# Kernel optimization log

Hardware: AMD Instinct MI355X
Metric: run time of the kernel (lower is better)

Reference implementation:

```python
import jax, jax.numpy as jnp
import numpy as np

NUM_HEADS = 16

def setup_inputs() -> dict:
    key = jax.random.key(0)
    k1, k2, k3, k4 = jax.random.split(key, 4)
    B, N, C = 4, 2048, 1024
    x = jax.random.normal(k1, (B, N, C), dtype=jnp.float32)
    xpos = jax.random.randint(k2, (B, N), 0, 2048, dtype=jnp.int64)
    Wqkv = jax.random.normal(k3, (C, 3 * C), dtype=jnp.float32) * (C ** -0.5)
    Wproj = jax.random.normal(k4, (C, C), dtype=jnp.float32) * (C ** -0.5)
    bproj = jnp.zeros((C,), dtype=jnp.float32)
    return {"x": x, "xpos": xpos, "Wqkv": Wqkv, "Wproj": Wproj, "bproj": bproj}

def reference(x, xpos, Wqkv, Wproj, bproj):
    # rope is None in this configuration, so xpos is unused (matches torch default path).
    B, N, C = x.shape
    H = NUM_HEADS
    Dh = C // H
    scale = Dh ** -0.5
    qkv = jnp.einsum('bnc,cd->bnd', x, Wqkv)              # [B, N, 3C]
    qkv = qkv.reshape(B, N, 3, H, Dh)
    q, k, v = qkv[:, :, 0], qkv[:, :, 1], qkv[:, :, 2]    # [B, N, H, Dh]
    scores = jnp.einsum('bnhd,bmhd->bhnm', q, k) * scale  # [B, H, N, N]
    attn = jax.nn.softmax(scores, axis=-1)
    out = jnp.einsum('bhnm,bmhd->bnhd', attn, v)          # [B, N, H, Dh]
    out = out.reshape(B, N, C)
    return jnp.einsum('bnc,cd->bnd', out, Wproj) + bproj
```

## Files before the change

kernel.cpp:

```cpp
#include <hip/hip_runtime.h>
#include <stdint.h>

#define DEVINL __device__ __forceinline__

typedef __bf16 bf16x8 __attribute__((ext_vector_type(8)));
typedef float f32x4 __attribute__((ext_vector_type(4)));
typedef float f32x16 __attribute__((ext_vector_type(16)));
typedef uint32_t u32x4 __attribute__((ext_vector_type(4)));

DEVINL uint16_t f2bf(float f) {
    uint32_t u = __builtin_bit_cast(uint32_t, f);
    uint32_t r = (u + 0x7FFFu + ((u >> 16) & 1u)) >> 16;
    return (uint16_t)r;
}

DEVINL bf16x8 ld8(const uint16_t* p) {
    u32x4 v = *(const u32x4*)p;
    return __builtin_bit_cast(bf16x8, v);
}

DEVINL void gload16(const void* g, void* l) {
    __builtin_amdgcn_global_load_lds(
        (const __attribute__((address_space(1))) uint32_t*)g,
        (__attribute__((address_space(3))) uint32_t*)l, 16, 0, 0);
}

DEVINL uint32_t cvtpk(float lo, float hi) {
    uint32_t r;
    asm("v_cvt_pk_bf16_f32 %0, %1, %2" : "=v"(r) : "v"(lo), "v"(hi));
    return r;
}

DEVINL float exp2_fast(float x) {
    float r;
    asm("v_exp_f32 %0, %1" : "=v"(r) : "v"(x));
    return r;
}

__global__ void k_cvt_x(const float* __restrict__ x, uint16_t* __restrict__ xb, int n8) {
    int i = blockIdx.x * blockDim.x + threadIdx.x;
    if (i >= n8) return;
    const float4* src = (const float4*)x + (size_t)i * 2;
    float4 a = src[0], b = src[1];
    union { uint16_t u[8]; u32x4 v; } o;
    o.u[0] = f2bf(a.x); o.u[1] = f2bf(a.y); o.u[2] = f2bf(a.z); o.u[3] = f2bf(a.w);
    o.u[4] = f2bf(b.x); o.u[5] = f2bf(b.y); o.u[6] = f2bf(b.z); o.u[7] = f2bf(b.w);
    ((u32x4*)xb)[i] = o.v;
}

__global__ void k_transW(const float* __restrict__ W, uint16_t* __restrict__ WT, int Nn) {
    __shared__ uint16_t t[64 * 65];
    int k0 = blockIdx.y * 64, n0 = blockIdx.x * 64;
    int tid = threadIdx.x;
#pragma unroll
    for (int i = 0; i < 4; ++i) {
        int c = tid + i * 256;
        int kr = c >> 4, nc = c & 15;
        float4 v = *(const float4*)(W + (size_t)(k0 + kr) * Nn + n0 + nc * 4);
        t[(nc * 4 + 0) * 65 + kr] = f2bf(v.x);
        t[(nc * 4 + 1) * 65 + kr] = f2bf(v.y);
        t[(nc * 4 + 2) * 65 + kr] = f2bf(v.z);
        t[(nc * 4 + 3) * 65 + kr] = f2bf(v.w);
    }
    __syncthreads();
#pragma unroll
    for (int i = 0; i < 2; ++i) {
        int c = tid + i * 256;
        int nr = c >> 3, kc = c & 7;
        union { uint16_t u[8]; u32x4 v; } o;
#pragma unroll
        for (int j = 0; j < 8; ++j) o.u[j] = t[nr * 65 + kc * 8 + j];
        *(u32x4*)(WT + (size_t)(n0 + nr) * 1024 + k0 + kc * 8) = o.v;
    }
}

__global__ void k_transV(const uint16_t* __restrict__ vn, uint16_t* __restrict__ vt) {
    __shared__ uint16_t t[64 * 65];
    int bh = blockIdx.y;
    int n0 = blockIdx.x * 64;
    int tid = threadIdx.x;
#pragma unroll
    for (int i = 0; i < 2; ++i) {
        int c = tid + i * 256;
        int n = c >> 3, dc = c & 7;
        u32x4 vv = *(const u32x4*)(vn + ((size_t)bh * 2048 + n0 + n) * 64 + dc * 8);
        union { u32x4 v4; uint16_t u[8]; } in; in.v4 = vv;
#pragma unroll
        for (int j = 0; j < 8; ++j) t[(dc * 8 + j) * 65 + n] = in.u[j];
    }
    __syncthreads();
#pragma unroll
    for (int i = 0; i < 2; ++i) {
        int c = tid + i * 256;
        int dh = c >> 3, nc = c & 7;
        union { uint16_t u[8]; u32x4 v4; } o;
#pragma unroll
        for (int j = 0; j < 8; ++j) o.u[j] = t[dh * 65 + nc * 8 + j];
        *(u32x4*)(vt + ((size_t)bh * 64 + dh) * 2048 + n0 + nc * 8) = o.v4;
    }
}

template <int MODE>
__global__ __launch_bounds__(256) void k_gemm(
    const uint16_t* __restrict__ A, const uint16_t* __restrict__ BT,
    const float* __restrict__ bias,
    uint16_t* __restrict__ qo, uint16_t* __restrict__ ko, uint16_t* __restrict__ vo,
    float* __restrict__ out) {
    __shared__ uint16_t a_lds[128 * 64];
    __shared__ uint16_t b_lds[128 * 64];
    int tid = threadIdx.x;
    int w = tid >> 6, l = tid & 63;
    int l15 = l & 15, l4 = l >> 4;
    int m0 = blockIdx.y * 128, n0 = blockIdx.x * 128;
    int wr = w >> 1, wc = w & 1;
    f32x4 acc[4][4] = {};

    for (int kt = 0; kt < 16; ++kt) {
#pragma unroll
        for (int i = 0; i < 4; ++i) {
            int c = i * 256 + w * 64 + l;
            int row = c >> 3, slot = c & 7;
            int kc = slot ^ (row & 7);
            gload16(A + (size_t)(m0 + row) * 1024 + kt * 64 + kc * 8,
                    a_lds + (size_t)(i * 256 + w * 64) * 8);
            gload16(BT + (size_t)(n0 + row) * 1024 + kt * 64 + kc * 8,
                    b_lds + (size_t)(i * 256 + w * 64) * 8);
        }
        __syncthreads();
#pragma unroll
        for (int kkk = 0; kkk < 2; ++kkk) {
            bf16x8 af[4], bfr[4];
#pragma unroll
            for (int i = 0; i < 4; ++i) {
                int row = wr * 64 + i * 16 + l15;
                af[i] = ld8(a_lds + row * 64 + ((kkk * 4 + l4) ^ (row & 7)) * 8);
                int rowb = wc * 64 + i * 16 + l15;
                bfr[i] = ld8(b_lds + rowb * 64 + ((kkk * 4 + l4) ^ (rowb & 7)) * 8);
            }
#pragma unroll
            for (int i = 0; i < 4; ++i)
#pragma unroll
                for (int j = 0; j < 4; ++j)
                    acc[i][j] = __builtin_amdgcn_mfma_f32_16x16x32_bf16(
                        af[i], bfr[j], acc[i][j], 0, 0, 0);
        }
        __syncthreads();
    }

    if constexpr (MODE == 0) {
#pragma unroll
        for (int i = 0; i < 4; ++i)
#pragma unroll
            for (int j = 0; j < 4; ++j) {
                int d = n0 + wc * 64 + j * 16 + l15;
                int s = d >> 10, h = (d >> 6) & 15, dh = d & 63;
                uint16_t* dst0 = (s == 0) ? qo : (s == 1) ? ko : vo;
                float sc = (s == 0) ? 0.18033688011112042f : 1.0f;
#pragma unroll
                for (int r = 0; r < 4; ++r) {
                    int m = m0 + wr * 64 + i * 16 + l4 * 4 + r;
                    int b = m >> 11, n = m & 2047;
                    dst0[((size_t)(b * 16 + h) * 2048 + n) * 64 + dh] = f2bf(acc[i][j][r] * sc);
                }
            }
    } else {
#pragma unroll
        for (int j = 0; j < 4; ++j) {
            int d = n0 + wc * 64 + j * 16 + l15;
            float bv = bias[d];
#pragma unroll
            for (int i = 0; i < 4; ++i)
#pragma unroll
                for (int r = 0; r < 4; ++r) {
                    int m = m0 + wr * 64 + i * 16 + l4 * 4 + r;
                    out[(size_t)m * 1024 + d] = acc[i][j][r] + bv;
                }
        }
    }
}

__global__ __launch_bounds__(256) void k_attn(
    const uint16_t* __restrict__ q, const uint16_t* __restrict__ kk_,
    const uint16_t* __restrict__ vt, uint16_t* __restrict__ o) {
    __shared__ uint16_t k_lds[2][64 * 64];
    __shared__ uint16_t v_lds[2][64 * 64];
    int tid = threadIdx.x;
    int w = tid >> 6, l = tid & 63;
    int l31 = l & 31, g = l >> 5;
    int bh = blockIdx.y;
    int qt = blockIdx.x;
    int qrow = qt * 128 + w * 32 + l31;
    const uint16_t* qb = q + ((size_t)bh * 2048 + qrow) * 64;
    const uint16_t* kbase = kk_ + (size_t)bh * 2048 * 64;
    const uint16_t* vbase = vt + (size_t)bh * 64 * 2048;

    bf16x8 qf[4];
#pragma unroll
    for (int kv = 0; kv < 4; ++kv) qf[kv] = ld8(qb + kv * 16 + g * 8);

    int c0 = w * 128 + l;
    int rr0 = c0 >> 3, sl0 = c0 & 7;
    int kc0 = sl0 ^ (rr0 & 7);
    int rr1 = rr0 + 8, kc1 = sl0 ^ (rr1 & 7);
    const uint16_t* kp0 = kbase + rr0 * 64 + kc0 * 8;
    const uint16_t* kp1 = kbase + rr1 * 64 + kc1 * 8;
    const uint16_t* vp0 = vbase + (size_t)rr0 * 2048 + kc0 * 8;
    const uint16_t* vp1 = vbase + (size_t)rr1 * 2048 + kc1 * 8;
    uint16_t* kd0 = k_lds[0] + w * 1024;
    uint16_t* kd1 = k_lds[1] + w * 1024;
    uint16_t* vd0 = v_lds[0] + w * 1024;
    uint16_t* vd1 = v_lds[1] + w * 1024;

    f32x16 oa[2] = {};
    f32x16 ls = {};
    u32x4 onesu; onesu[0] = onesu[1] = onesu[2] = onesu[3] = 0x3F803F80u;
    bf16x8 ones = __builtin_bit_cast(bf16x8, onesu);

    auto stage = [&](uint16_t* kd, uint16_t* vd) {
        gload16(kp0, kd);       gload16(kp1, kd + 512);
        gload16(vp0, vd);       gload16(vp1, vd + 512);
        kp0 += 4096; kp1 += 4096; vp0 += 64; vp1 += 64;
    };

    stage(kd0, vd0);
    asm volatile("s_waitcnt vmcnt(0)\n\ts_barrier" ::: "memory");

    auto body = [&](int t, const uint16_t* kb, const uint16_t* vb,
                    uint16_t* kdn, uint16_t* vdn) {
        if (t < 31) stage(kdn, vdn);

        bf16x8 pfrag[4];
#pragma unroll
        for (int j = 0; j < 2; ++j) {
            int key = j * 32 + l31;
            f32x16 stj = {};
            __builtin_amdgcn_s_setprio(1);
#pragma unroll
            for (int kv = 0; kv < 4; ++kv) {
                bf16x8 kf = ld8(kb + key * 64 + ((2 * kv + g) ^ (key & 7)) * 8);
                stj = __builtin_amdgcn_mfma_f32_32x32x16_bf16(kf, qf[kv], stj, 0, 0, 0);
            }
            __builtin_amdgcn_s_setprio(0);
#pragma unroll
            for (int h = 0; h < 2; ++h) {
                float e[8];
#pragma unroll
                for (int jj = 0; jj < 8; ++jj) e[jj] = exp2_fast(stj[h * 8 + jj]);
                uint32_t a0 = cvtpk(e[0], e[1]), a1 = cvtpk(e[2], e[3]);
                uint32_t b0 = cvtpk(e[4], e[5]), b1 = cvtpk(e[6], e[7]);
                auto r0 = __builtin_amdgcn_permlane32_swap(a0, b0, false, false);
                auto r1 = __builtin_amdgcn_permlane32_swap(a1, b1, false, false);
                u32x4 f;
                f[0] = r0[0]; f[1] = r1[0]; f[2] = r0[1]; f[3] = r1[1];
                pfrag[j * 2 + h] = __builtin_bit_cast(bf16x8, f);
            }
        }

        __builtin_amdgcn_s_setprio(1);
#pragma unroll
        for (int kv = 0; kv < 4; ++kv) {
            ls = __builtin_amdgcn_mfma_f32_32x32x16_bf16(ones, pfrag[kv], ls, 0, 0, 0);
#pragma unroll
            for (int dt = 0; dt < 2; ++dt) {
                int dh = dt * 32 + l31;
                bf16x8 vf = ld8(vb + dh * 64 + ((2 * kv + g) ^ (dh & 7)) * 8);
                oa[dt] = __builtin_amdgcn_mfma_f32_32x32x16_bf16(vf, pfrag[kv], oa[dt], 0, 0, 0);
            }
        }
        __builtin_amdgcn_s_setprio(0);
        asm volatile("s_waitcnt vmcnt(0)\n\ts_barrier" ::: "memory");
    };

    for (int kt = 0; kt < 32; kt += 2) {
        body(kt,     k_lds[0], v_lds[0], kd1, vd1);
        body(kt + 1, k_lds[1], v_lds[1], kd0, vd0);
    }

    float inv = 1.0f / ls[0];
    int b = bh >> 4, h = bh & 15;
    uint16_t* ob = o + ((size_t)(b * 2048 + qrow)) * 1024 + h * 64;
#pragma unroll
    for (int dt = 0; dt < 2; ++dt)
#pragma unroll
        for (int rq = 0; rq < 4; ++rq) {
            union { uint16_t u[4]; uint2 v; } pk;
#pragma unroll
            for (int rr = 0; rr < 4; ++rr) pk.u[rr] = f2bf(oa[dt][rq * 4 + rr] * inv);
            int dh0 = dt * 32 + rq * 8 + g * 4;
            *(uint2*)(ob + dh0) = pk.v;
        }
}

extern "C" void kernel_launch(void* const* d_in, const int* in_sizes, int n_in,
                              void* d_out, int out_size, void* d_ws, size_t ws_size,
                              hipStream_t stream) {
    const float* x     = (const float*)d_in[0];
    const float* Wqkv  = (const float*)d_in[2];
    const float* Wproj = (const float*)d_in[3];
    const float* bproj = (const float*)d_in[4];
    float* out = (float*)d_out;

    char* ws = (char*)d_ws;
    uint16_t* xb     = (uint16_t*)(ws);
    uint16_t* wqkvT  = (uint16_t*)(ws + 16777216);
    uint16_t* wprojT = (uint16_t*)(ws + 23068672);
    uint16_t* qws    = (uint16_t*)(ws + 25165824);
    uint16_t* kws    = (uint16_t*)(ws + 41943040);
    uint16_t* vT     = (uint16_t*)(ws + 58720256);
    uint16_t* vnat   = (uint16_t*)(ws + 75497472);
    uint16_t* attnout = xb;

    k_cvt_x<<<dim3(4096), dim3(256), 0, stream>>>(x, xb, 1048576);
    k_transW<<<dim3(48, 16), dim3(256), 0, stream>>>(Wqkv, wqkvT, 3072);
    k_transW<<<dim3(16, 16), dim3(256), 0, stream>>>(Wproj, wprojT, 1024);
    k_gemm<0><<<dim3(24, 64), dim3(256), 0, stream>>>(xb, wqkvT, nullptr, qws, kws, vnat, nullptr);
    k_transV<<<dim3(32, 64), dim3(256), 0, stream>>>(vnat, vT);
    k_attn<<<dim3(16, 64), dim3(256), 0, stream>>>(qws, kws, vT, attnout);
    k_gemm<1><<<dim3(8, 64), dim3(256), 0, stream>>>(attnout, wprojT, bproj, nullptr, nullptr, nullptr, out);
}
```

Baseline: 221.9 us.

## Fuse prep kernels, remap attention grid, split barriers, sum softmax denominators in VALU

Merges the x conversion and both weight transposes into one prep launch. Remaps attention blocks to a 1D grid so blocks sharing a head are spread across XCDs. Splits the single end-of-iteration wait into partial vmcnt waits, so K can be consumed while V is still loading. Replaces the ones-matrix MFMA used for the row-sum with a VALU accumulation plus a cross-half shuffle. The finer-grained waits depend on exact outstanding-load counts and add extra barriers.

```diff
diff --git a/kernel.cpp b/kernel.cpp
--- a/kernel.cpp
+++ b/kernel.cpp
@@ -37,21 +37,8 @@
     return r;
 }
 
-__global__ void k_cvt_x(const float* __restrict__ x, uint16_t* __restrict__ xb, int n8) {
-    int i = blockIdx.x * blockDim.x + threadIdx.x;
-    if (i >= n8) return;
-    const float4* src = (const float4*)x + (size_t)i * 2;
-    float4 a = src[0], b = src[1];
-    union { uint16_t u[8]; u32x4 v; } o;
-    o.u[0] = f2bf(a.x); o.u[1] = f2bf(a.y); o.u[2] = f2bf(a.z); o.u[3] = f2bf(a.w);
-    o.u[4] = f2bf(b.x); o.u[5] = f2bf(b.y); o.u[6] = f2bf(b.z); o.u[7] = f2bf(b.w);
-    ((u32x4*)xb)[i] = o.v;
-}
-
-__global__ void k_transW(const float* __restrict__ W, uint16_t* __restrict__ WT, int Nn) {
-    __shared__ uint16_t t[64 * 65];
-    int k0 = blockIdx.y * 64, n0 = blockIdx.x * 64;
-    int tid = threadIdx.x;
+DEVINL void transW_body(const float* __restrict__ W, uint16_t* __restrict__ WT,
+                        int Nn, int n0, int k0, int tid, uint16_t* t) {
 #pragma unroll
     for (int i = 0; i < 4; ++i) {
         int c = tid + i * 256;
@@ -71,6 +58,29 @@
 #pragma unroll
         for (int j = 0; j < 8; ++j) o.u[j] = t[nr * 65 + kc * 8 + j];
         *(u32x4*)(WT + (size_t)(n0 + nr) * 1024 + k0 + kc * 8) = o.v;
+    }
+}
+
+__global__ void k_prep(const float* __restrict__ x, uint16_t* __restrict__ xb,
+                       const float* __restrict__ Wqkv, uint16_t* __restrict__ wqkvT,
+                       const float* __restrict__ Wproj, uint16_t* __restrict__ wprojT) {
+    __shared__ uint16_t t[64 * 65];
+    int bid = blockIdx.x;
+    int tid = threadIdx.x;
+    if (bid < 4096) {
+        int i = bid * 256 + tid;
+        const float4* src = (const float4*)x + (size_t)i * 2;
+        float4 a = src[0], b = src[1];
+        union { uint16_t u[8]; u32x4 v; } o;
+        o.u[0] = f2bf(a.x); o.u[1] = f2bf(a.y); o.u[2] = f2bf(a.z); o.u[3] = f2bf(a.w);
+        o.u[4] = f2bf(b.x); o.u[5] = f2bf(b.y); o.u[6] = f2bf(b.z); o.u[7] = f2bf(b.w);
+        ((u32x4*)xb)[i] = o.v;
+    } else if (bid < 4864) {
+        int idx = bid - 4096;
+        transW_body(Wqkv, wqkvT, 3072, (idx % 48) * 64, (idx / 48) * 64, tid, t);
+    } else {
+        int idx = bid - 4864;
+        transW_body(Wproj, wprojT, 1024, (idx % 16) * 64, (idx / 16) * 64, tid, t);
     }
 }
 
@@ -187,8 +197,10 @@
     int tid = threadIdx.x;
     int w = tid >> 6, l = tid & 63;
     int l31 = l & 31, g = l >> 5;
-    int bh = blockIdx.y;
-    int qt = blockIdx.x;
+    int bid = blockIdx.x;
+    int slot = bid >> 3;
+    int bh = (bid & 7) * 8 + (slot >> 4);
+    int qt = slot & 15;
     int qrow = qt * 128 + w * 32 + l31;
     const uint16_t* qb = q + ((size_t)bh * 2048 + qrow) * 64;
     const uint16_t* kbase = kk_ + (size_t)bh * 2048 * 64;
@@ -212,9 +224,7 @@
     uint16_t* vd1 = v_lds[1] + w * 1024;
 
     f32x16 oa[2] = {};
-    f32x16 ls = {};
-    u32x4 onesu; onesu[0] = onesu[1] = onesu[2] = onesu[3] = 0x3F803F80u;
-    bf16x8 ones = __builtin_bit_cast(bf16x8, onesu);
+    float lsum = 0.f;
 
     auto stage = [&](uint16_t* kd, uint16_t* vd) {
         gload16(kp0, kd);       gload16(kp1, kd + 512);
@@ -223,10 +233,10 @@
     };
 
     stage(kd0, vd0);
-    asm volatile("s_waitcnt vmcnt(0)\n\ts_barrier" ::: "memory");
 
     auto body = [&](int t, const uint16_t* kb, const uint16_t* vb,
                     uint16_t* kdn, uint16_t* vdn) {
+        asm volatile("s_waitcnt vmcnt(2)\n\ts_barrier" ::: "memory");
         if (t < 31) stage(kdn, vdn);
 
         bf16x8 pfrag[4];
@@ -246,6 +256,7 @@
                 float e[8];
 #pragma unroll
                 for (int jj = 0; jj < 8; ++jj) e[jj] = exp2_fast(stj[h * 8 + jj]);
+                lsum += ((e[0] + e[1]) + (e[2] + e[3])) + ((e[4] + e[5]) + (e[6] + e[7]));
                 uint32_t a0 = cvtpk(e[0], e[1]), a1 = cvtpk(e[2], e[3]);
                 uint32_t b0 = cvtpk(e[4], e[5]), b1 = cvtpk(e[6], e[7]);
                 auto r0 = __builtin_amdgcn_permlane32_swap(a0, b0, false, false);
@@ -256,10 +267,12 @@
             }
         }
 
+        if (t < 31) asm volatile("s_waitcnt vmcnt(4)\n\ts_barrier" ::: "memory");
+        else        asm volatile("s_waitcnt vmcnt(0)\n\ts_barrier" ::: "memory");
+
         __builtin_amdgcn_s_setprio(1);
 #pragma unroll
         for (int kv = 0; kv < 4; ++kv) {
-            ls = __builtin_amdgcn_mfma_f32_32x32x16_bf16(ones, pfrag[kv], ls, 0, 0, 0);
 #pragma unroll
             for (int dt = 0; dt < 2; ++dt) {
                 int dh = dt * 32 + l31;
@@ -268,7 +281,6 @@
             }
         }
         __builtin_amdgcn_s_setprio(0);
-        asm volatile("s_waitcnt vmcnt(0)\n\ts_barrier" ::: "memory");
     };
 
     for (int kt = 0; kt < 32; kt += 2) {
@@ -276,7 +288,8 @@
         body(kt + 1, k_lds[1], v_lds[1], kd0, vd0);
     }
 
-    float inv = 1.0f / ls[0];
+    float ltot = lsum + __shfl_xor(lsum, 32, 64);
+    float inv = 1.0f / ltot;
     int b = bh >> 4, h = bh & 15;
     uint16_t* ob = o + ((size_t)(b * 2048 + qrow)) * 1024 + h * 64;
 #pragma unroll
@@ -310,11 +323,9 @@
     uint16_t* vnat   = (uint16_t*)(ws + 75497472);
     uint16_t* attnout = xb;
 
-    k_cvt_x<<<dim3(4096), dim3(256), 0, stream>>>(x, xb, 1048576);
-    k_transW<<<dim3(48, 16), dim3(256), 0, stream>>>(Wqkv, wqkvT, 3072);
-    k_transW<<<dim3(16, 16), dim3(256), 0, stream>>>(Wproj, wprojT, 1024);
+    k_prep<<<dim3(5120), dim3(256), 0, stream>>>(x, xb, Wqkv, wqkvT, Wproj, wprojT);
     k_gemm<0><<<dim3(24, 64), dim3(256), 0, stream>>>(xb, wqkvT, nullptr, qws, kws, vnat, nullptr);
     k_transV<<<dim3(32, 64), dim3(256), 0, stream>>>(vnat, vT);
-    k_attn<<<dim3(16, 64), dim3(256), 0, stream>>>(qws, kws, vT, attnout);
+    k_attn<<<dim3(1024), dim3(256), 0, stream>>>(qws, kws, vT, attnout);
     k_gemm<1><<<dim3(8, 64), dim3(256), 0, stream>>>(attnout, wprojT, bproj, nullptr, nullptr, nullptr, out);
 }
```

After: 211.1 us. 1.05x faster.
